# Kernel tuning notes

Measured on AMD Instinct MI355X. Metric: run time of the kernel, lower is better.

## Reference

```python
import jax, jax.numpy as jnp
import numpy as np

ROPE_BASE = 10000.0
NEG = -1e9

def _rope_tables(N, head_dim, dtype):
    # freq buffer: angles[pos, i] = pos / base^(2i/head_dim), i over half dim
    inv = 1.0 / (ROPE_BASE ** (jnp.arange(0, head_dim, 2, dtype=jnp.float32) / head_dim))
    ang = jnp.arange(N, dtype=jnp.float32)[:, None] * inv[None, :]  # (N, hd/2)
    return jnp.cos(ang).astype(dtype), jnp.sin(ang).astype(dtype)

def _apply_rope(t, cos, sin):
    # t: (B, h, N, hd); rotate-half style
    hd = t.shape[-1]
    t1, t2 = t[..., : hd // 2], t[..., hd // 2 :]
    c = cos[None, None]  # (1,1,N,hd/2)
    s = sin[None, None]
    return jnp.concatenate([t1 * c - t2 * s, t1 * s + t2 * c], axis=-1)


def setup_inputs() -> dict:
    key = jax.random.key(0)
    B, N, D, h = 2, 2048, 2048, 16
    ks = jax.random.split(key, 5)
    x = jax.random.normal(ks[0], (B, N, D), dtype=jnp.float32)
    Wqkv = jax.random.normal(ks[1], (3 * D, D), dtype=jnp.float32) * 0.02
    Wproj = jax.random.normal(ks[2], (D, D), dtype=jnp.float32) * 0.02
    bproj = jax.random.normal(ks[3], (D,), dtype=jnp.float32) * 0.02
    L = jax.random.randint(ks[4], (B,), 1, N + 1, dtype=jnp.int32)
    return {"x": x, "Wqkv": Wqkv, "Wproj": Wproj, "bproj": bproj, "L": L, "n_heads": 16}


def reference(x, Wqkv, Wproj, bproj, L, n_heads):
    B, N, D = x.shape
    hd = D // n_heads
    scale = 1.0 / jnp.sqrt(jnp.asarray(hd, dtype=x.dtype))

    # fused QKV projection (no bias)
    qkv = jnp.einsum('bnd,ed->bne', x, Wqkv)  # (B, N, 3D)
    q, k, v = jnp.split(qkv, 3, axis=-1)
    # (B, N, h*hd) -> (B, h, N, hd)
    def heads(t):
        return t.reshape(B, N, n_heads, hd).transpose(0, 2, 1, 3)
    q, k, v = heads(q), heads(k), heads(v)

    cos, sin = _rope_tables(N, hd, x.dtype)
    q = _apply_rope(q, cos, sin)
    k = _apply_rope(k, cos, sin)

    # causal + key-padding mask (pos < L valid)
    pos = jnp.arange(N)
    causal = pos[:, None] >= pos[None, :]                    # (N, N)
    key_valid = pos[None, :] < L[:, None]                    # (B, N)
    mask = causal[None, None] & key_valid[:, None, None, :]  # (B,1,N,N)

    scores = jnp.einsum('bhqd,bhkd->bhqk', q, k) * scale
    scores = jnp.where(mask, scores, NEG)
    attn = jax.nn.softmax(scores, axis=-1)
    out = jnp.einsum('bhqk,bhkd->bhqd', attn, v)             # (B,h,N,hd)
    out = out.transpose(0, 2, 1, 3).reshape(B, N, D)
    return jnp.einsum('bnd,ed->bne', out, Wproj) + bproj
```

## Files before the change

kernel.cpp:

```cpp
#include <hip/hip_runtime.h>
#include <hip/hip_bf16.h>


typedef unsigned short u16;
typedef short bf16x8 __attribute__((ext_vector_type(8)));
typedef unsigned short u16x8 __attribute__((ext_vector_type(8)));
typedef float f32x4 __attribute__((ext_vector_type(4)));

#define MFMA16(a, b, c) __builtin_amdgcn_mfma_f32_16x16x32_bf16((a), (b), (c), 0, 0, 0)

__device__ __forceinline__ float b2f(u16 u) { return __uint_as_float(((unsigned)u) << 16); }
__device__ __forceinline__ u16 f2b(float f) {
    unsigned x = __float_as_uint(f);
    return (u16)((x + 0x7fffu + ((x >> 16) & 1u)) >> 16);
}
__device__ __forceinline__ void gload16(const u16* g, u16* lds) {
    __builtin_amdgcn_global_load_lds((__attribute__((address_space(1))) void*)g,
                                     (__attribute__((address_space(3))) void*)lds,
                                     16, 0, 0);
}

__global__ __launch_bounds__(256) void cvt_bf16(const float* __restrict__ in,
                                                u16* __restrict__ out) {
    size_t i = (size_t)blockIdx.x * 256 + threadIdx.x;
    float4 a = ((const float4*)in)[2 * i];
    float4 b = ((const float4*)in)[2 * i + 1];
    u16x8 o;
    o[0] = f2b(a.x); o[1] = f2b(a.y); o[2] = f2b(a.z); o[3] = f2b(a.w);
    o[4] = f2b(b.x); o[5] = f2b(b.y); o[6] = f2b(b.z); o[7] = f2b(b.w);
    ((u16x8*)out)[i] = o;
}

__global__ __launch_bounds__(256) void rope_tables_k(float* __restrict__ cosT,
                                                     float* __restrict__ sinT) {
    int idx = blockIdx.x * 256 + threadIdx.x;
    int n = idx >> 6, i = idx & 63;
    float inv = powf(10000.0f, -(float)(2 * i) / 128.0f);
    float ang = (float)n * inv;
    cosT[idx] = cosf(ang);
    sinT[idx] = sinf(ang);
}

__global__ __launch_bounds__(256, 2) void gemm1_fused(
    const u16* __restrict__ A, const u16* __restrict__ B,
    const float* __restrict__ cosT, const float* __restrict__ sinT,
    u16* __restrict__ Q, u16* __restrict__ Ko, u16* __restrict__ VT) {
    __shared__ u16 smem[17408];
    u16* As = smem;
    u16* Bs = smem + 8192;
    const int K = 2048;
    const int tx = threadIdx.x;
    const int w = tx >> 6, l = tx & 63;
    const int fr = l & 15, fg = l >> 4;
    const int wr = w >> 1, wc = w & 1;
    const long row0 = (long)blockIdx.x * 128;
    const long col0 = (long)blockIdx.y * 128;
    f32x4 acc[4][4] = {};
    int rs[4], ss[4];
#pragma unroll
    for (int i = 0; i < 4; ++i) {
        int c = i * 256 + tx;
        rs[i] = c >> 3;
        ss[i] = (c & 7) ^ ((c >> 3) & 7);
    }
    for (int kt = 0; kt < 32; ++kt) {
        const long k0 = (long)kt << 6;
        __syncthreads();
#pragma unroll
        for (int i = 0; i < 4; ++i)
            gload16(A + (row0 + rs[i]) * K + k0 + ss[i] * 8, &As[(i * 256 + w * 64) * 8]);
#pragma unroll
        for (int i = 0; i < 4; ++i)
            gload16(B + (col0 + rs[i]) * K + k0 + ss[i] * 8, &Bs[(i * 256 + w * 64) * 8]);
        __syncthreads();
#pragma unroll
        for (int kk = 0; kk < 2; ++kk) {
            bf16x8 af[4], bfv[4];
#pragma unroll
            for (int m = 0; m < 4; ++m) {
                int r = wr * 64 + m * 16 + fr;
                af[m] = *(const bf16x8*)&As[r * 64 + (((kk * 4 + fg) ^ (r & 7)) << 3)];
            }
#pragma unroll
            for (int n = 0; n < 4; ++n) {
                int r = wc * 64 + n * 16 + fr;
                bfv[n] = *(const bf16x8*)&Bs[r * 64 + (((kk * 4 + fg) ^ (r & 7)) << 3)];
            }
#pragma unroll
            for (int m = 0; m < 4; ++m)
#pragma unroll
                for (int n = 0; n < 4; ++n) acc[m][n] = MFMA16(af[m], bfv[n], acc[m][n]);
        }
    }
    const int sec = blockIdx.y >> 4;
    const int h = blockIdx.y & 15;
    const int b = (int)(row0 >> 11);
    const int n0 = (int)(row0 & 2047);
    const int bh = b * 16 + h;
    __syncthreads();
#pragma unroll
    for (int m = 0; m < 4; ++m)
#pragma unroll
        for (int n = 0; n < 4; ++n)
#pragma unroll
            for (int r = 0; r < 4; ++r)
                smem[(wr * 64 + m * 16 + fg * 4 + r) * 136 + wc * 64 + n * 16 + fr] =
                    f2b(acc[m][n][r]);
    __syncthreads();
    if (sec < 2) {
        const float SC = (sec == 0) ? 0.08838834764831844f : 1.0f;
        u16* dstb = (sec == 0 ? Q : Ko) + ((size_t)bh * 2048 + n0) * 128;
#pragma unroll
        for (int i = 0; i < 4; ++i) {
            int cid = i * 256 + tx;
            int rowl = cid >> 3, g = cid & 7;
            int d0 = g * 8;
            int ntok = n0 + rowl;
            u16x8 t1 = *(const u16x8*)&smem[rowl * 136 + d0];
            u16x8 t2 = *(const u16x8*)&smem[rowl * 136 + 64 + d0];
            float4 c1 = *(const float4*)&cosT[ntok * 64 + d0];
            float4 c2 = *(const float4*)&cosT[ntok * 64 + d0 + 4];
            float4 s1 = *(const float4*)&sinT[ntok * 64 + d0];
            float4 s2 = *(const float4*)&sinT[ntok * 64 + d0 + 4];
            float cc[8] = {c1.x, c1.y, c1.z, c1.w, c2.x, c2.y, c2.z, c2.w};
            float ssn[8] = {s1.x, s1.y, s1.z, s1.w, s2.x, s2.y, s2.z, s2.w};
            u16x8 o1, o2;
#pragma unroll
            for (int j = 0; j < 8; ++j) {
                float a = b2f(t1[j]), bb = b2f(t2[j]);
                o1[j] = f2b((a * cc[j] - bb * ssn[j]) * SC);
                o2[j] = f2b((a * ssn[j] + bb * cc[j]) * SC);
            }
            *(u16x8*)&dstb[(size_t)rowl * 128 + d0] = o1;
            *(u16x8*)&dstb[(size_t)rowl * 128 + 64 + d0] = o2;
        }
    } else {
#pragma unroll
        for (int i = 0; i < 8; ++i) {
            int cid = i * 256 + tx;
            int d = cid >> 4, g = cid & 15;
            u16x8 o;
#pragma unroll
            for (int e = 0; e < 8; ++e) o[e] = smem[(g * 8 + e) * 136 + d];
            *(u16x8*)&VT[((size_t)bh * 128 + d) * 2048 + n0 + g * 8] = o;
        }
    }
}

__global__ __launch_bounds__(256, 2) void gemm_nt_f32(const u16* __restrict__ A,
                                                      const u16* __restrict__ B,
                                                      float* __restrict__ C,
                                                      const float* __restrict__ bias,
                                                      int Ncols, int K) {
    __shared__ u16 As[128 * 64];
    __shared__ u16 Bs[128 * 64];
    const int tx = threadIdx.x;
    const int w = tx >> 6, l = tx & 63;
    const int fr = l & 15, fg = l >> 4;
    const int wr = w >> 1, wc = w & 1;
    const long row0 = (long)blockIdx.x * 128;
    const long col0 = (long)blockIdx.y * 128;
    f32x4 acc[4][4] = {};
    const int nk = K >> 6;
    int rs[4], ss[4];
#pragma unroll
    for (int i = 0; i < 4; ++i) {
        int c = i * 256 + tx;
        rs[i] = c >> 3;
        ss[i] = (c & 7) ^ ((c >> 3) & 7);
    }
    for (int kt = 0; kt < nk; ++kt) {
        const long k0 = (long)kt << 6;
        __syncthreads();
#pragma unroll
        for (int i = 0; i < 4; ++i)
            gload16(A + (row0 + rs[i]) * K + k0 + ss[i] * 8, &As[(i * 256 + w * 64) * 8]);
#pragma unroll
        for (int i = 0; i < 4; ++i)
            gload16(B + (col0 + rs[i]) * K + k0 + ss[i] * 8, &Bs[(i * 256 + w * 64) * 8]);
        __syncthreads();
#pragma unroll
        for (int kk = 0; kk < 2; ++kk) {
            bf16x8 af[4], bfv[4];
#pragma unroll
            for (int m = 0; m < 4; ++m) {
                int r = wr * 64 + m * 16 + fr;
                af[m] = *(const bf16x8*)&As[r * 64 + (((kk * 4 + fg) ^ (r & 7)) << 3)];
            }
#pragma unroll
            for (int n = 0; n < 4; ++n) {
                int r = wc * 64 + n * 16 + fr;
                bfv[n] = *(const bf16x8*)&Bs[r * 64 + (((kk * 4 + fg) ^ (r & 7)) << 3)];
            }
#pragma unroll
            for (int m = 0; m < 4; ++m)
#pragma unroll
                for (int n = 0; n < 4; ++n) acc[m][n] = MFMA16(af[m], bfv[n], acc[m][n]);
        }
    }
#pragma unroll
    for (int m = 0; m < 4; ++m)
#pragma unroll
        for (int n = 0; n < 4; ++n)
#pragma unroll
            for (int r = 0; r < 4; ++r) {
                long row = row0 + wr * 64 + m * 16 + fg * 4 + r;
                long col = col0 + wc * 64 + n * 16 + fr;
                C[row * Ncols + col] = acc[m][n][r] + bias[col];
            }
}

__global__ __launch_bounds__(256, 2) void attn_k(const u16* __restrict__ Q,
                                                 const u16* __restrict__ K,
                                                 const u16* __restrict__ VT,
                                                 u16* __restrict__ O,
                                                 const int* __restrict__ L) {
    const int bh = blockIdx.y, b = bh >> 4, h = bh & 15;
    const int qx = blockIdx.x;
    const int qb0 = qx << 6, qb1 = (31 - qx) << 6;
    const int tx = threadIdx.x;
    const int w = tx >> 6, l = tx & 63;
    const int fr = l & 15, fg = l >> 4;
    const int Lb = L[b];
    __shared__ u16 Ks[2][64 * 128];
    __shared__ u16 Vs[2][128 * 64];
    __shared__ u16 Ps[4][16 * 72];
    const u16* Qh = Q + (size_t)bh * 2048 * 128;
    const u16* Kh = K + (size_t)bh * 2048 * 128;
    const u16* Vh = VT + (size_t)bh * 128 * 2048;
    bf16x8 aq0[4], aq1[4];
#pragma unroll
    for (int kc = 0; kc < 4; ++kc) {
        aq0[kc] = *(const bf16x8*)&Qh[(size_t)(qb0 + w * 16 + fr) * 128 + kc * 32 + fg * 8];
        aq1[kc] = *(const bf16x8*)&Qh[(size_t)(qb1 + w * 16 + fr) * 128 + kc * 32 + fg * 8];
    }
    f32x4 accO0[8] = {}, accO1[8] = {};
    float mr0[4] = {-1e30f, -1e30f, -1e30f, -1e30f};
    float mr1[4] = {-1e30f, -1e30f, -1e30f, -1e30f};
    float sr0[4] = {0.f, 0.f, 0.f, 0.f};
    float sr1[4] = {0.f, 0.f, 0.f, 0.f};
    const int kmax = min(qb1 + 63, Lb - 1);
    const int nkt = (kmax >> 6) + 1;

    auto stage_tile = [&](int kt0, int buf) {
#pragma unroll
        for (int i = 0; i < 4; ++i) {
            int c = i * 256 + tx;
            int row = c >> 4, cp = c & 15;
            gload16(Kh + (size_t)(kt0 + row) * 128 + ((cp ^ (row & 7)) << 3),
                    &Ks[buf][(i * 256 + w * 64) * 8]);
        }
#pragma unroll
        for (int i = 0; i < 4; ++i) {
            int c = i * 256 + tx;
            int row = c >> 3, cp = c & 7;
            gload16(Vh + (size_t)row * 2048 + kt0 + ((cp ^ (row & 7)) << 3),
                    &Vs[buf][(i * 256 + w * 64) * 8]);
        }
    };

    auto do_strip = [&](const bf16x8 (&aqs)[4], float (&mr)[4], float (&sr)[4],
                        f32x4 (&aO)[8], int qgb, int kt0, const u16* Ksb,
                        const u16* Vsb) {
        f32x4 accS[4];
#pragma unroll
        for (int st = 0; st < 4; ++st) {
            f32x4 z = {0.f, 0.f, 0.f, 0.f};
            accS[st] = z;
            int key = st * 16 + fr;
#pragma unroll
            for (int kc = 0; kc < 4; ++kc) {
                bf16x8 bk = *(const bf16x8*)&Ksb[key * 128 + (((kc * 4 + fg) ^ (key & 7)) << 3)];
                accS[st] = MFMA16(aqs[kc], bk, accS[st]);
            }
        }
        float sv[4][4];
        if ((kt0 + 63 <= qgb) && (kt0 + 63 < Lb)) {
#pragma unroll
            for (int st = 0; st < 4; ++st)
#pragma unroll
                for (int r = 0; r < 4; ++r) sv[st][r] = accS[st][r];
        } else {
#pragma unroll
            for (int st = 0; st < 4; ++st)
#pragma unroll
                for (int r = 0; r < 4; ++r) {
                    int key = kt0 + st * 16 + fr;
                    int qg = qgb + fg * 4 + r;
                    sv[st][r] = (key <= qg && key < Lb) ? accS[st][r] : -1e30f;
                }
        }
        float alpha[4], pr[4][4];
#pragma unroll
        for (int r = 0; r < 4; ++r) {
            float lm = fmaxf(fmaxf(sv[0][r], sv[1][r]), fmaxf(sv[2][r], sv[3][r]));
            lm = fmaxf(lm, __shfl_xor(lm, 1));
            lm = fmaxf(lm, __shfl_xor(lm, 2));
            lm = fmaxf(lm, __shfl_xor(lm, 4));
            lm = fmaxf(lm, __shfl_xor(lm, 8));
            float mn = fmaxf(mr[r], lm);
            alpha[r] = exp2f((mr[r] - mn) * 1.44269504f);
            float ls = 0.f;
#pragma unroll
            for (int st = 0; st < 4; ++st) {
                float p = exp2f((sv[st][r] - mn) * 1.44269504f);
                pr[st][r] = p;
                ls += p;
            }
            ls += __shfl_xor(ls, 1);
            ls += __shfl_xor(ls, 2);
            ls += __shfl_xor(ls, 4);
            ls += __shfl_xor(ls, 8);
            sr[r] = sr[r] * alpha[r] + ls;
            mr[r] = mn;
        }
#pragma unroll
        for (int n = 0; n < 8; ++n)
#pragma unroll
            for (int r = 0; r < 4; ++r) aO[n][r] *= alpha[r];
#pragma unroll
        for (int st = 0; st < 4; ++st)
#pragma unroll
            for (int r = 0; r < 4; ++r)
                Ps[w][(fg * 4 + r) * 72 + st * 16 + fr] = f2b(pr[st][r]);
#pragma unroll
        for (int ks = 0; ks < 2; ++ks) {
            bf16x8 ap = *(const bf16x8*)&Ps[w][fr * 72 + ks * 32 + fg * 8];
#pragma unroll
            for (int n = 0; n < 8; ++n) {
                int d = n * 16 + fr;
                bf16x8 bv = *(const bf16x8*)&Vsb[d * 64 + (((ks * 4 + fg) ^ (d & 7)) << 3)];
                aO[n] = MFMA16(ap, bv, aO[n]);
            }
        }
    };

    stage_tile(0, 0);
    int cur = 0;
    for (int kt = 0; kt < nkt; ++kt) {
        const int kt0 = kt << 6;
        __syncthreads();
        if (kt + 1 < nkt) stage_tile((kt + 1) << 6, cur ^ 1);
        if (kt <= qx)
            do_strip(aq0, mr0, sr0, accO0, qb0 + w * 16, kt0, Ks[cur], Vs[cur]);
        do_strip(aq1, mr1, sr1, accO1, qb1 + w * 16, kt0, Ks[cur], Vs[cur]);
        cur ^= 1;
    }
    float inv0[4], inv1[4];
#pragma unroll
    for (int r = 0; r < 4; ++r) {
        inv0[r] = 1.0f / sr0[r];
        inv1[r] = 1.0f / sr1[r];
    }
#pragma unroll
    for (int n = 0; n < 8; ++n)
#pragma unroll
        for (int r = 0; r < 4; ++r) {
            int d = n * 16 + fr;
            int q0 = qb0 + w * 16 + fg * 4 + r;
            int q1 = qb1 + w * 16 + fg * 4 + r;
            O[((size_t)(b * 2048 + q0)) * 2048 + h * 128 + d] = f2b(accO0[n][r] * inv0[r]);
            O[((size_t)(b * 2048 + q1)) * 2048 + h * 128 + d] = f2b(accO1[n][r] * inv1[r]);
        }
}

extern "C" void kernel_launch(void* const* d_in, const int* in_sizes, int n_in,
                              void* d_out, int out_size, void* d_ws, size_t ws_size,
                              hipStream_t stream) {
    const float* x = (const float*)d_in[0];
    const float* Wqkv = (const float*)d_in[1];
    const float* Wproj = (const float*)d_in[2];
    const float* bproj = (const float*)d_in[3];
    const int* L = (const int*)d_in[4];
    float* out = (float*)d_out;

    char* p = (char*)d_ws;
    u16* xbf = (u16*)(p + 0);
    u16* wqkvbf = (u16*)(p + 16777216);
    u16* wprojbf = (u16*)(p + 41943040);
    u16* Qb = (u16*)(p + 50331648);
    u16* Kb = (u16*)(p + 100663296);
    u16* VTb = (u16*)(p + 117440512);
    float* cosT = (float*)(p + 134217728);
    float* sinT = (float*)(p + 134742016);
    u16* Ob = xbf;

    cvt_bf16<<<4096, 256, 0, stream>>>(x, xbf);
    cvt_bf16<<<6144, 256, 0, stream>>>(Wqkv, wqkvbf);
    cvt_bf16<<<2048, 256, 0, stream>>>(Wproj, wprojbf);
    rope_tables_k<<<512, 256, 0, stream>>>(cosT, sinT);
    gemm1_fused<<<dim3(32, 48), 256, 0, stream>>>(xbf, wqkvbf, cosT, sinT, Qb, Kb, VTb);
    attn_k<<<dim3(16, 32), 256, 0, stream>>>(Qb, Kb, VTb, Ob, L);
    gemm_nt_f32<<<dim3(32, 16), 256, 0, stream>>>(Ob, wprojbf, out, bproj, 2048, 2048);
}
```

Measured before the change: 245.5 us.

## Share V fragment loads across both query strips and swizzle P buffer

The attention loop now runs QK and softmax for both query strips first, then runs a single PV pass that reuses each V fragment read from LDS for both strips' MFMAs. This halves V shared-memory reads whenever both strips are active. The P buffer grows to 32 rows per wave and uses an XOR swizzle instead of padding to avoid bank conflicts. Separately, the QKV epilogue writes V transposed into shared memory, so the VT store becomes a single vector LDS read instead of eight scalar gathers. Holding both strips' accumulators and two P fragments live raises register pressure.

```diff
diff --git a/kernel.cpp b/kernel.cpp
--- a/kernel.cpp
+++ b/kernel.cpp
@@ -98,16 +98,16 @@
     const int n0 = (int)(row0 & 2047);
     const int bh = b * 16 + h;
     __syncthreads();
-#pragma unroll
-    for (int m = 0; m < 4; ++m)
-#pragma unroll
-        for (int n = 0; n < 4; ++n)
-#pragma unroll
-            for (int r = 0; r < 4; ++r)
-                smem[(wr * 64 + m * 16 + fg * 4 + r) * 136 + wc * 64 + n * 16 + fr] =
-                    f2b(acc[m][n][r]);
-    __syncthreads();
     if (sec < 2) {
+#pragma unroll
+        for (int m = 0; m < 4; ++m)
+#pragma unroll
+            for (int n = 0; n < 4; ++n)
+#pragma unroll
+                for (int r = 0; r < 4; ++r)
+                    smem[(wr * 64 + m * 16 + fg * 4 + r) * 136 + wc * 64 + n * 16 + fr] =
+                        f2b(acc[m][n][r]);
+        __syncthreads();
         const float SC = (sec == 0) ? 0.08838834764831844f : 1.0f;
         u16* dstb = (sec == 0 ? Q : Ko) + ((size_t)bh * 2048 + n0) * 128;
 #pragma unroll
@@ -136,13 +136,20 @@
         }
     } else {
 #pragma unroll
+        for (int m = 0; m < 4; ++m)
+#pragma unroll
+            for (int n = 0; n < 4; ++n)
+#pragma unroll
+                for (int r = 0; r < 4; ++r)
+                    smem[(wc * 64 + n * 16 + fr) * 136 + wr * 64 + m * 16 + fg * 4 + r] =
+                        f2b(acc[m][n][r]);
+        __syncthreads();
+#pragma unroll
         for (int i = 0; i < 8; ++i) {
             int cid = i * 256 + tx;
             int d = cid >> 4, g = cid & 15;
-            u16x8 o;
-#pragma unroll
-            for (int e = 0; e < 8; ++e) o[e] = smem[(g * 8 + e) * 136 + d];
-            *(u16x8*)&VT[((size_t)bh * 128 + d) * 2048 + n0 + g * 8] = o;
+            *(u16x8*)&VT[((size_t)bh * 128 + d) * 2048 + n0 + g * 8] =
+                *(const u16x8*)&smem[d * 136 + g * 8];
         }
     }
 }
@@ -224,7 +231,7 @@
     const int Lb = L[b];
     __shared__ u16 Ks[2][64 * 128];
     __shared__ u16 Vs[2][128 * 64];
-    __shared__ u16 Ps[4][16 * 72];
+    __shared__ u16 Ps[4][32 * 64];
     const u16* Qh = Q + (size_t)bh * 2048 * 128;
     const u16* Kh = K + (size_t)bh * 2048 * 128;
     const u16* Vh = VT + (size_t)bh * 128 * 2048;
@@ -259,10 +266,7 @@
         }
     };
 
-    auto do_strip = [&](const bf16x8 (&aqs)[4], float (&mr)[4], float (&sr)[4],
-                        f32x4 (&aO)[8], int qgb, int kt0, const u16* Ksb,
-                        const u16* Vsb) {
-        f32x4 accS[4];
+    auto do_qk = [&](const bf16x8 (&aqs)[4], f32x4 (&accS)[4], const u16* Ksb) {
 #pragma unroll
         for (int st = 0; st < 4; ++st) {
             f32x4 z = {0.f, 0.f, 0.f, 0.f};
@@ -274,6 +278,10 @@
                 accS[st] = MFMA16(aqs[kc], bk, accS[st]);
             }
         }
+    };
+
+    auto softmax_store = [&](f32x4 (&accS)[4], float (&mr)[4], float (&sr)[4],
+                             f32x4 (&aO)[8], int qgb, int kt0, int prow) {
         float sv[4][4];
         if ((kt0 + 63 <= qgb) && (kt0 + 63 < Lb)) {
 #pragma unroll
@@ -321,18 +329,11 @@
 #pragma unroll
         for (int st = 0; st < 4; ++st)
 #pragma unroll
-            for (int r = 0; r < 4; ++r)
-                Ps[w][(fg * 4 + r) * 72 + st * 16 + fr] = f2b(pr[st][r]);
-#pragma unroll
-        for (int ks = 0; ks < 2; ++ks) {
-            bf16x8 ap = *(const bf16x8*)&Ps[w][fr * 72 + ks * 32 + fg * 8];
-#pragma unroll
-            for (int n = 0; n < 8; ++n) {
-                int d = n * 16 + fr;
-                bf16x8 bv = *(const bf16x8*)&Vsb[d * 64 + (((ks * 4 + fg) ^ (d & 7)) << 3)];
-                aO[n] = MFMA16(ap, bv, aO[n]);
-            }
-        }
+            for (int r = 0; r < 4; ++r) {
+                int e = st * 16 + fr;
+                int row = prow + fg * 4 + r;
+                Ps[w][row * 64 + (((e >> 3) ^ (row & 7)) << 3) + (e & 7)] = f2b(pr[st][r]);
+            }
     };
 
     stage_tile(0, 0);
@@ -341,9 +342,48 @@
         const int kt0 = kt << 6;
         __syncthreads();
         if (kt + 1 < nkt) stage_tile((kt + 1) << 6, cur ^ 1);
-        if (kt <= qx)
-            do_strip(aq0, mr0, sr0, accO0, qb0 + w * 16, kt0, Ks[cur], Vs[cur]);
-        do_strip(aq1, mr1, sr1, accO1, qb1 + w * 16, kt0, Ks[cur], Vs[cur]);
+        const u16* Ksb = Ks[cur];
+        const u16* Vsb = Vs[cur];
+        if (kt <= qx) {
+            {
+                f32x4 s[4];
+                do_qk(aq0, s, Ksb);
+                softmax_store(s, mr0, sr0, accO0, qb0 + w * 16, kt0, 0);
+            }
+            {
+                f32x4 s[4];
+                do_qk(aq1, s, Ksb);
+                softmax_store(s, mr1, sr1, accO1, qb1 + w * 16, kt0, 16);
+            }
+#pragma unroll
+            for (int ks = 0; ks < 2; ++ks) {
+                bf16x8 ap0 = *(const bf16x8*)&Ps[w][fr * 64 + (((ks * 4 + fg) ^ (fr & 7)) << 3)];
+                bf16x8 ap1 =
+                    *(const bf16x8*)&Ps[w][(16 + fr) * 64 + (((ks * 4 + fg) ^ (fr & 7)) << 3)];
+#pragma unroll
+                for (int n = 0; n < 8; ++n) {
+                    int d = n * 16 + fr;
+                    bf16x8 bv = *(const bf16x8*)&Vsb[d * 64 + (((ks * 4 + fg) ^ (d & 7)) << 3)];
+                    accO0[n] = MFMA16(ap0, bv, accO0[n]);
+                    accO1[n] = MFMA16(ap1, bv, accO1[n]);
+                }
+            }
+        } else {
+            f32x4 s[4];
+            do_qk(aq1, s, Ksb);
+            softmax_store(s, mr1, sr1, accO1, qb1 + w * 16, kt0, 16);
+#pragma unroll
+            for (int ks = 0; ks < 2; ++ks) {
+                bf16x8 ap1 =
+                    *(const bf16x8*)&Ps[w][(16 + fr) * 64 + (((ks * 4 + fg) ^ (fr & 7)) << 3)];
+#pragma unroll
+                for (int n = 0; n < 8; ++n) {
+                    int d = n * 16 + fr;
+                    bf16x8 bv = *(const bf16x8*)&Vsb[d * 64 + (((ks * 4 + fg) ^ (d & 7)) << 3)];
+                    accO1[n] = MFMA16(ap1, bv, accO1[n]);
+                }
+            }
+        }
         cur ^= 1;
     }
     float inv0[4], inv1[4];
```

Result: slower. 392.7 us (+59.9%).
